# Performance work log

Hardware: AMD Instinct MI355X
Metric: run time of the kernel (lower is better)

The kernel has to match this reference:

```python
import jax, jax.numpy as jnp
import numpy as np

B, N, D = 4, 2048, 2048
HEADS, KV_HEADS = 16, 4
DH = D // HEADS            # 128 per-head dim
KV_RATIO = HEADS // KV_HEADS
MAX_LEN, MAX_BSZ = 2048, 4
EPS = 1.1920929e-07        # torch.finfo(float32).eps (RMSNorm default eps=None)


def _rot_tables(n, d, base=10000.0):
    thetas = base ** (-jnp.arange(0, d, 2, dtype=jnp.float32) / d)   # [d/2]
    ang = jnp.arange(n, dtype=jnp.float32)[:, None] * thetas[None, :]
    cos = jnp.repeat(jnp.cos(ang), 2, axis=-1)   # [n, d] interleaved pairs
    sin = jnp.repeat(jnp.sin(ang), 2, axis=-1)
    return cos, sin


def _rotate_half_inverted(x):
    x1 = x[..., ::2]
    x2 = x[..., 1::2]
    return jnp.stack([-x2, x1], axis=-1).reshape(x.shape)


def _apply_rotation(x, end, start=0):
    cos, sin = _rot_tables(MAX_LEN, DH)
    return x * cos[start:end] + _rotate_half_inverted(x) * sin[start:end]


def setup_inputs() -> dict:
    key = jax.random.key(0)
    ks = jax.random.split(key, 4)
    s = 0.02
    return {
        "x": jax.random.normal(ks[0], (B, N, D), jnp.float32),
        "norm_w": jnp.ones((D,), jnp.float32),
        "qw": jax.random.normal(ks[1], (HEADS * DH, D), jnp.float32) * s,
        "qb": jnp.zeros((HEADS * DH,), jnp.float32),
        "kvw": jax.random.normal(ks[2], (2 * DH * KV_HEADS, D), jnp.float32) * s,
        "kvb": jnp.zeros((2 * DH * KV_HEADS,), jnp.float32),
        "wow": jax.random.normal(ks[3], (D, HEADS * DH), jnp.float32) * s,
        "wob": jnp.zeros((D,), jnp.float32),
        "kv_cache": jnp.zeros((MAX_BSZ, MAX_LEN, 2 * DH * KV_HEADS), jnp.float32),
        "pos": 0,
    }


def reference(x, norm_w, qw, qb, kvw, kvb, wow, wob, kv_cache, pos):
    b, n, d = x.shape
    t = pos + n  # total cached length
    # RMSNorm
    xn = x * jax.lax.rsqrt(jnp.mean(x * x, axis=-1, keepdims=True) + EPS) * norm_w
    # Q projection -> [b, heads, n, dh]
    q = (xn @ qw.T + qb).reshape(b, n, HEADS, DH).transpose(0, 2, 1, 3)
    # KV projection + cache write/read
    kv = xn @ kvw.T + kvb                                  # [b, n, 2*dh*kv_heads]
    cache = jax.lax.dynamic_update_slice(kv_cache, kv, (0, pos, 0))
    kvf = cache[:b, :t].reshape(b, t, KV_HEADS, 2 * DH).transpose(0, 2, 1, 3)
    kvf = jnp.repeat(kvf, KV_RATIO, axis=1)                # GQA expand -> [b, heads, t, 2dh]
    k, v = kvf[..., :DH], kvf[..., DH:]
    # RoPE (interleaved-pair variant)
    q = _apply_rotation(q, t, pos)
    k = _apply_rotation(k, t, 0)
    # Attention (decoder causal)
    attn = jnp.einsum("bhqd,bhkd->bhqk", q, k) / jnp.sqrt(jnp.float32(DH))
    if n > 1:
        mask = jnp.triu(jnp.ones((n, t), bool), k=1 + pos)
        attn = jnp.where(mask, -jnp.inf, attn)
    attn = jax.nn.softmax(attn, axis=-1)
    o = jnp.einsum("bhqk,bhkd->bhqd", attn, v).transpose(0, 2, 1, 3).reshape(b, n, HEADS * DH)
    return o @ wow.T + wob
```

## Files before the change

### kernel.cpp

```cpp
#include <hip/hip_runtime.h>
#include <hip/hip_bf16.h>

typedef unsigned short u16;
typedef unsigned int u32;
typedef __attribute__((ext_vector_type(4))) float f32x4;
typedef __attribute__((ext_vector_type(8))) short s16x8;

#define B_ 4
#define N_ 2048
#define D_ 2048
#define HEADS_ 16
#define KVH_ 4
#define DH_ 128
#define KVD_ 1024
#define M_ 8192
#define SCALE_ 0.08838834764831845f

__device__ __forceinline__ u16 f2bf(float f) {
  u32 u = __builtin_bit_cast(u32, f);
  return (u16)((u + 0x7FFFu + ((u >> 16) & 1u)) >> 16);
}

__device__ __forceinline__ void gload_lds16(const void* g, void* l) {
  __builtin_amdgcn_global_load_lds(
      (const __attribute__((address_space(1))) u32*)g,
      (__attribute__((address_space(3))) u32*)l, 16, 0, 0);
}

__global__ __launch_bounds__(256)
void rope_tab_k(float* __restrict__ cost, float* __restrict__ sint)
{
  const int idx = blockIdx.x * 256 + threadIdx.x;
  const int p = idx >> 6, i = idx & 63;
  const float theta = expf(-(float)i * 0.015625f * 9.210340371976184f);
  float s, c;
  sincosf((float)p * theta, &s, &c);
  cost[idx] = c;
  sint[idx] = s;
}

__global__ __launch_bounds__(256)
void cvt_bf16_k(const float* __restrict__ s, u16* __restrict__ d, int n)
{
  const int i = (blockIdx.x * 256 + threadIdx.x) * 8;
  if (i >= n) return;
  const f32x4 a = *(const f32x4*)(s + i);
  const f32x4 b = *(const f32x4*)(s + i + 4);
  s16x8 o;
  #pragma unroll
  for (int j = 0; j < 4; ++j) { o[j] = (short)f2bf(a[j]); o[4 + j] = (short)f2bf(b[j]); }
  *(s16x8*)(d + i) = o;
}

__global__ __launch_bounds__(256)
void rmsnorm_k(const float* __restrict__ x, const float* __restrict__ w, u16* __restrict__ xn)
{
  const int row = blockIdx.x, t = threadIdx.x;
  const float* xr = x + (size_t)row * D_;
  const f32x4 a = *(const f32x4*)(xr + t * 8);
  const f32x4 b = *(const f32x4*)(xr + t * 8 + 4);
  float ss = a[0]*a[0] + a[1]*a[1] + a[2]*a[2] + a[3]*a[3]
           + b[0]*b[0] + b[1]*b[1] + b[2]*b[2] + b[3]*b[3];
  #pragma unroll
  for (int off = 32; off >= 1; off >>= 1) ss += __shfl_xor(ss, off);
  __shared__ float wss[4];
  if ((t & 63) == 0) wss[t >> 6] = ss;
  __syncthreads();
  const float tot = wss[0] + wss[1] + wss[2] + wss[3];
  const float rs = rsqrtf(tot * (1.0f / D_) + 1.1920929e-07f);
  s16x8 o;
  #pragma unroll
  for (int j = 0; j < 4; ++j) {
    o[j]     = (short)f2bf(a[j] * rs * w[t * 8 + j]);
    o[4 + j] = (short)f2bf(b[j] * rs * w[t * 8 + 4 + j]);
  }
  *(s16x8*)(xn + (size_t)row * D_ + t * 8) = o;
}

template<int EPI>
__global__ __launch_bounds__(256)
void gemm_bt(const u16* __restrict__ A, const u16* __restrict__ Bw,
             void* __restrict__ Cv, const float* __restrict__ bias,
             int N, int K,
             const float* __restrict__ cos_t, const float* __restrict__ sin_t)
{
  __shared__ u16 As[128 * 32];
  __shared__ u16 Bs[128 * 32];
  const int t = threadIdx.x;
  const int w = t >> 6, lane = t & 63;
  const int g = lane >> 4, lr = lane & 15;
  const int row0 = blockIdx.x * 128, col0 = blockIdx.y * 128;
  const int wr = (w >> 1) * 64, wc = (w & 1) * 64;

  f32x4 acc[4][4] = {};

  const u16* gA = A + (size_t)(row0 + w * 16 + (lane >> 2)) * K + (lane & 3) * 8;
  const u16* gB = Bw + (size_t)(col0 + w * 16 + (lane >> 2)) * K + (lane & 3) * 8;
  u16* lA = As + (w * 16) * 32;
  u16* lB = Bs + (w * 16) * 32;

  for (int kt = 0; kt < K; kt += 32) {
    #pragma unroll
    for (int r = 0; r < 2; ++r) {
      gload_lds16(gA + (size_t)(r * 64) * K + kt, lA + r * 64 * 32);
      gload_lds16(gB + (size_t)(r * 64) * K + kt, lB + r * 64 * 32);
    }
    __syncthreads();
    s16x8 af[4], bf[4];
    #pragma unroll
    for (int i = 0; i < 4; ++i) {
      af[i] = *(const s16x8*)(As + (wr + i * 16 + lr) * 32 + g * 8);
      bf[i] = *(const s16x8*)(Bs + (wc + i * 16 + lr) * 32 + g * 8);
    }
    #pragma unroll
    for (int mi = 0; mi < 4; ++mi)
      #pragma unroll
      for (int ni = 0; ni < 4; ++ni)
        acc[mi][ni] = __builtin_amdgcn_mfma_f32_16x16x32_bf16(af[mi], bf[ni], acc[mi][ni], 0, 0, 0);
    __syncthreads();
  }

  #pragma unroll
  for (int mi = 0; mi < 4; ++mi) {
    #pragma unroll
    for (int ni = 0; ni < 4; ++ni) {
      const int cc = col0 + wc + ni * 16 + lr;
      const float bv = bias[cc];
      #pragma unroll
      for (int j = 0; j < 4; ++j) {
        const int rr = row0 + wr + mi * 16 + g * 4 + j;
        float v = acc[mi][ni][j] + bv;
        if (EPI == 0) {
          ((float*)Cv)[(size_t)rr * N + cc] = v;
        } else if (EPI == 1) {
          ((u16*)Cv)[(size_t)rr * N + cc] = f2bf(v);
        } else if (EPI == 2) {
          const int pos = rr & (N_ - 1);
          const int d = cc & (DH_ - 1);
          const float pv = __shfl_xor(v, 1);
          const float c = cos_t[pos * 64 + (d >> 1)];
          const float s = sin_t[pos * 64 + (d >> 1)];
          const float o = (d & 1) ? fmaf(v, c, pv * s) : fmaf(v, c, -pv * s);
          ((u16*)Cv)[(size_t)rr * N + cc] = f2bf(o);
        } else {
          const int pos = rr & (N_ - 1);
          const int dm = cc & 255;
          const float pv = __shfl_xor(v, 1);
          float o = v;
          if (dm < DH_) {
            const float c = cos_t[pos * 64 + (dm >> 1)];
            const float s = sin_t[pos * 64 + (dm >> 1)];
            o = (dm & 1) ? fmaf(v, c, pv * s) : fmaf(v, c, -pv * s);
          }
          ((u16*)Cv)[(size_t)rr * N + cc] = f2bf(o);
        }
      }
    }
  }
}

__global__ __launch_bounds__(256)
void vtrans_k(const u16* __restrict__ kvb, u16* __restrict__ vt)
{
  __shared__ u16 tile[64][65];
  const int z = blockIdx.z, b = z >> 2, kh = z & 3;
  const int p0 = blockIdx.x * 64, d0 = blockIdx.y * 64;
  const int t = threadIdx.x;
  #pragma unroll
  for (int r = 0; r < 2; ++r) {
    const int pl = r * 32 + (t >> 3), dl = (t & 7) * 8;
    const s16x8 v = *(const s16x8*)(kvb + (size_t)(b * N_ + p0 + pl) * KVD_ + kh * 256 + 128 + d0 + dl);
    #pragma unroll
    for (int jj = 0; jj < 8; ++jj) tile[pl][dl + jj] = (u16)v[jj];
  }
  __syncthreads();
  #pragma unroll
  for (int r = 0; r < 2; ++r) {
    const int dl = r * 32 + (t >> 3), pl = (t & 7) * 8;
    s16x8 o;
    #pragma unroll
    for (int jj = 0; jj < 8; ++jj) o[jj] = (short)tile[pl + jj][dl];
    *(s16x8*)(vt + ((size_t)(z * DH_ + d0 + dl)) * N_ + p0 + pl) = o;
  }
}

__global__ __launch_bounds__(512, 2)
void attn_k(const u16* __restrict__ q, const u16* __restrict__ kvb,
            const u16* __restrict__ vt, u16* __restrict__ out)
{
  const int fi = blockIdx.x, h = blockIdx.y, b = blockIdx.z;
  const int kh = h >> 2;
  const int t = threadIdx.x, w = t >> 6, lane = t & 63;
  const int g = lane >> 4, lr = lane & 15;

  __shared__ __align__(16) u16 Ks[2][64 * 128];
  __shared__ __align__(16) u16 Vs[2][128 * 64];
  __shared__ __align__(16) u16 Ps[8][16 * 64];

  const int kc = 2 * w;
  const int kr0 = kc * 4 + (lane >> 4);
  const int ksw0 = (lane & 15) ^ (kr0 & 7);
  const int kr1 = kr0 + 4;
  const int ksw1 = (lane & 15) ^ (kr1 & 7);
  const int vd0 = kc * 8 + (lane >> 3);
  const int vsw0 = (lane & 7) ^ (vd0 & 7);
  const int vd1 = vd0 + 8;
  const int vsw1 = (lane & 7) ^ (vd1 & 7);

  const u16* kbase = kvb + (size_t)b * (N_ * KVD_) + kh * 256;
  const u16* vbase = vt + (size_t)((b * KVH_ + kh) * DH_) * N_;

  int cur = 0;

  auto issue = [&](int kt, int buf) {
    gload_lds16(kbase + (size_t)(kt * 64 + kr0) * KVD_ + ksw0 * 8, &Ks[buf][kc * 512]);
    gload_lds16(kbase + (size_t)(kt * 64 + kr1) * KVD_ + ksw1 * 8, &Ks[buf][(kc + 1) * 512]);
    gload_lds16(vbase + (size_t)vd0 * N_ + kt * 64 + vsw0 * 8, &Vs[buf][kc * 512]);
    gload_lds16(vbase + (size_t)vd1 * N_ + kt * 64 + vsw1 * 8, &Vs[buf][(kc + 1) * 512]);
  };

  auto run_qtile = [&](int qi, int nkt, bool chain) {
    const int qrow0 = qi * 128 + w * 16;
    s16x8 qf[4];
    {
      const u16* qp = q + (size_t)(b * N_ + qrow0 + lr) * D_ + h * DH_;
      #pragma unroll
      for (int ks = 0; ks < 4; ++ks) qf[ks] = *(const s16x8*)(qp + ks * 32 + g * 8);
    }
    f32x4 o_acc[8] = {};
    float m_j[4], l_j[4];
    #pragma unroll
    for (int j = 0; j < 4; ++j) { m_j[j] = -1e30f; l_j[j] = 0.0f; }

    for (int kt = 0; kt < nkt; ++kt) {
      __syncthreads();
      if (kt + 1 < nkt)      issue(kt + 1, cur ^ 1);
      else if (chain)        issue(0, cur ^ 1);

      const u16* Kc = &Ks[cur][0];
      const u16* Vc = &Vs[cur][0];

      f32x4 sf[4] = {};
      #pragma unroll
      for (int ks = 0; ks < 4; ++ks) {
        #pragma unroll
        for (int kvf = 0; kvf < 4; ++kvf) {
          const int kvr = kvf * 16 + lr;
          const int ba = (kvr * 256 + ks * 64 + g * 16) ^ ((kvr & 7) << 4);
          const s16x8 kf = *(const s16x8*)((const char*)Kc + ba);
          sf[kvf] = __builtin_amdgcn_mfma_f32_16x16x32_bf16(qf[ks], kf, sf[kvf], 0, 0, 0);
        }
      }

      float pfac[4];
      #pragma unroll
      for (int j = 0; j < 4; ++j) {
        float mx = m_j[j];
        #pragma unroll
        for (int kvf = 0; kvf < 4; ++kvf) {
          float sv = sf[kvf][j] * SCALE_;
          const int kj = kt * 64 + kvf * 16 + lr;
          const int qi_row = qrow0 + g * 4 + j;
          if (kj > qi_row) sv = -1e30f;
          sf[kvf][j] = sv;
          mx = fmaxf(mx, sv);
        }
        mx = fmaxf(mx, __shfl_xor(mx, 1));
        mx = fmaxf(mx, __shfl_xor(mx, 2));
        mx = fmaxf(mx, __shfl_xor(mx, 4));
        mx = fmaxf(mx, __shfl_xor(mx, 8));
        pfac[j] = __expf(m_j[j] - mx);
        m_j[j] = mx;
      }
      #pragma unroll
      for (int df = 0; df < 8; ++df)
        #pragma unroll
        for (int j = 0; j < 4; ++j) o_acc[df][j] *= pfac[j];
      #pragma unroll
      for (int j = 0; j < 4; ++j) {
        float sum = 0.0f;
        #pragma unroll
        for (int kvf = 0; kvf < 4; ++kvf) {
          const float p = __expf(sf[kvf][j] - m_j[j]);
          sf[kvf][j] = p;
          sum += p;
        }
        sum += __shfl_xor(sum, 1);
        sum += __shfl_xor(sum, 2);
        sum += __shfl_xor(sum, 4);
        sum += __shfl_xor(sum, 8);
        l_j[j] = l_j[j] * pfac[j] + sum;
      }

      #pragma unroll
      for (int kvf = 0; kvf < 4; ++kvf)
        #pragma unroll
        for (int j = 0; j < 4; ++j) {
          const int rq = g * 4 + j, ck = kvf * 16 + lr;
          const int ba = (rq * 128 + ck * 2) ^ ((rq & 7) << 4);
          *(u16*)((char*)&Ps[w][0] + ba) = f2bf(sf[kvf][j]);
        }

      #pragma unroll
      for (int kk = 0; kk < 2; ++kk) {
        const int bap = (lr * 128 + kk * 64 + g * 16) ^ ((lr & 7) << 4);
        const s16x8 pf = *(const s16x8*)((const char*)&Ps[w][0] + bap);
        #pragma unroll
        for (int df = 0; df < 8; ++df) {
          const int dd = df * 16 + lr;
          const int bav = (dd * 128 + kk * 64 + g * 16) ^ ((dd & 7) << 4);
          const s16x8 vf = *(const s16x8*)((const char*)Vc + bav);
          o_acc[df] = __builtin_amdgcn_mfma_f32_16x16x32_bf16(pf, vf, o_acc[df], 0, 0, 0);
        }
      }
      cur ^= 1;
    }

    float inv_l[4];
    #pragma unroll
    for (int j = 0; j < 4; ++j) inv_l[j] = 1.0f / l_j[j];
    u16* op = out + (size_t)(b * N_ + qrow0) * D_ + h * DH_;
    #pragma unroll
    for (int df = 0; df < 8; ++df)
      #pragma unroll
      for (int j = 0; j < 4; ++j)
        op[(size_t)(g * 4 + j) * D_ + df * 16 + lr] = f2bf(o_acc[df][j] * inv_l[j]);
  };

  const int qlo = fi, qhi = 15 - fi;
  issue(0, 0);
  run_qtile(qlo, 2 * qlo + 2, true);
  run_qtile(qhi, 2 * qhi + 2, false);
}

extern "C" void kernel_launch(void* const* d_in, const int* in_sizes, int n_in,
                              void* d_out, int out_size, void* d_ws, size_t ws_size,
                              hipStream_t stream) {
  const float* x      = (const float*)d_in[0];
  const float* normw  = (const float*)d_in[1];
  const float* qw     = (const float*)d_in[2];
  const float* qbias  = (const float*)d_in[3];
  const float* kvw    = (const float*)d_in[4];
  const float* kvbias = (const float*)d_in[5];
  const float* wow    = (const float*)d_in[6];
  const float* wob    = (const float*)d_in[7];
  float* out = (float*)d_out;

  char* ws = (char*)d_ws;
  u16* xn    = (u16*)(ws + 0);
  u16* dq    = (u16*)(ws + 33554432);
  u16* dkv   = (u16*)(ws + 67108864);
  u16* dvt   = (u16*)(ws + 83886080);
  u16* qwb   = (u16*)(ws + 92274688);
  u16* kvwb  = (u16*)(ws + 100663296);
  u16* wowb  = (u16*)(ws + 104857600);
  float* cost = (float*)(ws + 113246208);
  float* sint = (float*)(ws + 113770496);

  rope_tab_k<<<512, 256, 0, stream>>>(cost, sint);
  cvt_bf16_k<<<2048, 256, 0, stream>>>(qw, qwb, 2048 * 2048);
  cvt_bf16_k<<<1024, 256, 0, stream>>>(kvw, kvwb, 1024 * 2048);
  cvt_bf16_k<<<2048, 256, 0, stream>>>(wow, wowb, 2048 * 2048);
  rmsnorm_k<<<8192, 256, 0, stream>>>(x, normw, xn);
  gemm_bt<2><<<dim3(64, 16), 256, 0, stream>>>(xn, qwb, (void*)dq, qbias, 2048, 2048, cost, sint);
  gemm_bt<3><<<dim3(64, 8), 256, 0, stream>>>(xn, kvwb, (void*)dkv, kvbias, 1024, 2048, cost, sint);
  vtrans_k<<<dim3(32, 2, 16), 256, 0, stream>>>(dkv, dvt);
  attn_k<<<dim3(8, 16, 4), 512, 0, stream>>>(dq, dkv, dvt, xn);
  gemm_bt<0><<<dim3(64, 16), 256, 0, stream>>>(xn, wowb, (void*)out, wob, 2048, 2048, nullptr, nullptr);
}
```

Baseline: 495.5 us.

## Fuse Q and KV projections into one GEMM and streamline attention softmax

```diff
diff --git a/kernel.cpp b/kernel.cpp
--- a/kernel.cpp
+++ b/kernel.cpp
@@ -15,10 +15,19 @@
 #define KVD_ 1024
 #define M_ 8192
 #define SCALE_ 0.08838834764831845f
+#define QSCALE2_ 0.12753257518622628f
 
 __device__ __forceinline__ u16 f2bf(float f) {
   u32 u = __builtin_bit_cast(u32, f);
   return (u16)((u + 0x7FFFu + ((u >> 16) & 1u)) >> 16);
+}
+
+__device__ __forceinline__ float fexp2(float x) {
+#if __has_builtin(__builtin_amdgcn_exp2f)
+  return __builtin_amdgcn_exp2f(x);
+#else
+  return exp2f(x);
+#endif
 }
 
 __device__ __forceinline__ void gload_lds16(const void* g, void* l) {
@@ -80,7 +89,8 @@
 template<int EPI>
 __global__ __launch_bounds__(256)
 void gemm_bt(const u16* __restrict__ A, const u16* __restrict__ Bw,
-             void* __restrict__ Cv, const float* __restrict__ bias,
+             void* __restrict__ Cv, void* __restrict__ Cv2,
+             const float* __restrict__ bias, const float* __restrict__ bias2,
              int N, int K,
              const float* __restrict__ cos_t, const float* __restrict__ sin_t)
 {
@@ -125,34 +135,33 @@
     #pragma unroll
     for (int ni = 0; ni < 4; ++ni) {
       const int cc = col0 + wc + ni * 16 + lr;
-      const float bv = bias[cc];
+      const float bv = (EPI == 4 && cc >= 2048) ? bias2[cc - 2048] : bias[cc];
       #pragma unroll
       for (int j = 0; j < 4; ++j) {
         const int rr = row0 + wr + mi * 16 + g * 4 + j;
         float v = acc[mi][ni][j] + bv;
         if (EPI == 0) {
-          ((float*)Cv)[(size_t)rr * N + cc] = v;
-        } else if (EPI == 1) {
-          ((u16*)Cv)[(size_t)rr * N + cc] = f2bf(v);
-        } else if (EPI == 2) {
-          const int pos = rr & (N_ - 1);
-          const int d = cc & (DH_ - 1);
-          const float pv = __shfl_xor(v, 1);
-          const float c = cos_t[pos * 64 + (d >> 1)];
-          const float s = sin_t[pos * 64 + (d >> 1)];
-          const float o = (d & 1) ? fmaf(v, c, pv * s) : fmaf(v, c, -pv * s);
-          ((u16*)Cv)[(size_t)rr * N + cc] = f2bf(o);
+          ((float*)Cv)[(size_t)rr * 2048 + cc] = v;
         } else {
           const int pos = rr & (N_ - 1);
-          const int dm = cc & 255;
           const float pv = __shfl_xor(v, 1);
-          float o = v;
-          if (dm < DH_) {
-            const float c = cos_t[pos * 64 + (dm >> 1)];
-            const float s = sin_t[pos * 64 + (dm >> 1)];
-            o = (dm & 1) ? fmaf(v, c, pv * s) : fmaf(v, c, -pv * s);
-          }
-          ((u16*)Cv)[(size_t)rr * N + cc] = f2bf(o);
+          if (cc < 2048) {
+            const int d = cc & (DH_ - 1);
+            const float c = cos_t[pos * 64 + (d >> 1)];
+            const float s = sin_t[pos * 64 + (d >> 1)];
+            const float o = (cc & 1) ? fmaf(v, c, pv * s) : fmaf(v, c, -pv * s);
+            ((u16*)Cv)[(size_t)rr * 2048 + cc] = f2bf(o);
+          } else {
+            const int ccc = cc - 2048;
+            const int dm = ccc & 255;
+            float o = v;
+            if (dm < DH_) {
+              const float c = cos_t[pos * 64 + (dm >> 1)];
+              const float s = sin_t[pos * 64 + (dm >> 1)];
+              o = (dm & 1) ? fmaf(v, c, pv * s) : fmaf(v, c, -pv * s);
+            }
+            ((u16*)Cv2)[(size_t)rr * 1024 + ccc] = f2bf(o);
+          }
         }
       }
     }
@@ -221,6 +230,7 @@
 
   auto run_qtile = [&](int qi, int nkt, bool chain) {
     const int qrow0 = qi * 128 + w * 16;
+    const int td = qrow0 >> 6;
     s16x8 qf[4];
     {
       const u16* qp = q + (size_t)(b * N_ + qrow0 + lr) * D_ + h * DH_;
@@ -237,88 +247,103 @@
       if (kt + 1 < nkt)      issue(kt + 1, cur ^ 1);
       else if (chain)        issue(0, cur ^ 1);
 
-      const u16* Kc = &Ks[cur][0];
-      const u16* Vc = &Vs[cur][0];
-
-      f32x4 sf[4] = {};
-      #pragma unroll
-      for (int ks = 0; ks < 4; ++ks) {
+      if (kt <= td) {
+        const u16* Kc = &Ks[cur][0];
+        const u16* Vc = &Vs[cur][0];
+
+        f32x4 sf[4] = {};
+        __builtin_amdgcn_s_setprio(1);
         #pragma unroll
-        for (int kvf = 0; kvf < 4; ++kvf) {
-          const int kvr = kvf * 16 + lr;
-          const int ba = (kvr * 256 + ks * 64 + g * 16) ^ ((kvr & 7) << 4);
-          const s16x8 kf = *(const s16x8*)((const char*)Kc + ba);
-          sf[kvf] = __builtin_amdgcn_mfma_f32_16x16x32_bf16(qf[ks], kf, sf[kvf], 0, 0, 0);
-        }
-      }
-
-      float pfac[4];
-      #pragma unroll
-      for (int j = 0; j < 4; ++j) {
-        float mx = m_j[j];
-        #pragma unroll
-        for (int kvf = 0; kvf < 4; ++kvf) {
-          float sv = sf[kvf][j] * SCALE_;
-          const int kj = kt * 64 + kvf * 16 + lr;
-          const int qi_row = qrow0 + g * 4 + j;
-          if (kj > qi_row) sv = -1e30f;
-          sf[kvf][j] = sv;
-          mx = fmaxf(mx, sv);
-        }
-        mx = fmaxf(mx, __shfl_xor(mx, 1));
-        mx = fmaxf(mx, __shfl_xor(mx, 2));
-        mx = fmaxf(mx, __shfl_xor(mx, 4));
-        mx = fmaxf(mx, __shfl_xor(mx, 8));
-        pfac[j] = __expf(m_j[j] - mx);
-        m_j[j] = mx;
-      }
-      #pragma unroll
-      for (int df = 0; df < 8; ++df)
-        #pragma unroll
-        for (int j = 0; j < 4; ++j) o_acc[df][j] *= pfac[j];
-      #pragma unroll
-      for (int j = 0; j < 4; ++j) {
-        float sum = 0.0f;
-        #pragma unroll
-        for (int kvf = 0; kvf < 4; ++kvf) {
-          const float p = __expf(sf[kvf][j] - m_j[j]);
-          sf[kvf][j] = p;
-          sum += p;
-        }
-        sum += __shfl_xor(sum, 1);
-        sum += __shfl_xor(sum, 2);
-        sum += __shfl_xor(sum, 4);
-        sum += __shfl_xor(sum, 8);
-        l_j[j] = l_j[j] * pfac[j] + sum;
-      }
-
-      #pragma unroll
-      for (int kvf = 0; kvf < 4; ++kvf)
+        for (int ks = 0; ks < 4; ++ks) {
+          #pragma unroll
+          for (int kvf = 0; kvf < 4; ++kvf) {
+            const int kvr = kvf * 16 + lr;
+            const int ba = (kvr * 256 + ks * 64 + g * 16) ^ ((kvr & 7) << 4);
+            const s16x8 kf = *(const s16x8*)((const char*)Kc + ba);
+            sf[kvf] = __builtin_amdgcn_mfma_f32_16x16x32_bf16(qf[ks], kf, sf[kvf], 0, 0, 0);
+          }
+        }
+        __builtin_amdgcn_s_setprio(0);
+
+        const bool need_mask = (kt == td);
+        float pmax[4];
         #pragma unroll
         for (int j = 0; j < 4; ++j) {
-          const int rq = g * 4 + j, ck = kvf * 16 + lr;
-          const int ba = (rq * 128 + ck * 2) ^ ((rq & 7) << 4);
-          *(u16*)((char*)&Ps[w][0] + ba) = f2bf(sf[kvf][j]);
-        }
-
-      #pragma unroll
-      for (int kk = 0; kk < 2; ++kk) {
-        const int bap = (lr * 128 + kk * 64 + g * 16) ^ ((lr & 7) << 4);
-        const s16x8 pf = *(const s16x8*)((const char*)&Ps[w][0] + bap);
+          float mx = -1e30f;
+          #pragma unroll
+          for (int kvf = 0; kvf < 4; ++kvf) {
+            float sv = sf[kvf][j] * QSCALE2_;
+            if (need_mask) {
+              const int kj = kt * 64 + kvf * 16 + lr;
+              const int qi_row = qrow0 + g * 4 + j;
+              if (kj > qi_row) sv = -1e30f;
+            }
+            sf[kvf][j] = sv;
+            mx = fmaxf(mx, sv);
+          }
+          mx = fmaxf(mx, __shfl_xor(mx, 1));
+          mx = fmaxf(mx, __shfl_xor(mx, 2));
+          mx = fmaxf(mx, __shfl_xor(mx, 4));
+          mx = fmaxf(mx, __shfl_xor(mx, 8));
+          pmax[j] = mx;
+        }
+
+        const float needv = fmaxf(fmaxf(pmax[0] - m_j[0], pmax[1] - m_j[1]),
+                                  fmaxf(pmax[2] - m_j[2], pmax[3] - m_j[3]));
+        if (__any(needv > 8.0f)) {
+          #pragma unroll
+          for (int j = 0; j < 4; ++j) {
+            const float mn = fmaxf(m_j[j], pmax[j]);
+            const float pf = fexp2(m_j[j] - mn);
+            m_j[j] = mn;
+            l_j[j] *= pf;
+            #pragma unroll
+            for (int df = 0; df < 8; ++df) o_acc[df][j] *= pf;
+          }
+        }
+
         #pragma unroll
-        for (int df = 0; df < 8; ++df) {
-          const int dd = df * 16 + lr;
-          const int bav = (dd * 128 + kk * 64 + g * 16) ^ ((dd & 7) << 4);
-          const s16x8 vf = *(const s16x8*)((const char*)Vc + bav);
-          o_acc[df] = __builtin_amdgcn_mfma_f32_16x16x32_bf16(pf, vf, o_acc[df], 0, 0, 0);
-        }
+        for (int j = 0; j < 4; ++j) {
+          float lacc = 0.0f;
+          #pragma unroll
+          for (int kvf = 0; kvf < 4; ++kvf) {
+            const float p = fexp2(sf[kvf][j] - m_j[j]);
+            lacc += p;
+            const int rq = g * 4 + j, ck = kvf * 16 + lr;
+            const int ba = (rq * 128 + ck * 2) ^ ((rq & 7) << 4);
+            *(u16*)((char*)&Ps[w][0] + ba) = (u16)(__builtin_bit_cast(u32, p) >> 16);
+          }
+          l_j[j] += lacc;
+        }
+
+        __builtin_amdgcn_s_setprio(1);
+        #pragma unroll
+        for (int kk = 0; kk < 2; ++kk) {
+          const int bap = (lr * 128 + kk * 64 + g * 16) ^ ((lr & 7) << 4);
+          const s16x8 pf = *(const s16x8*)((const char*)&Ps[w][0] + bap);
+          #pragma unroll
+          for (int df = 0; df < 8; ++df) {
+            const int dd = df * 16 + lr;
+            const int bav = (dd * 128 + kk * 64 + g * 16) ^ ((dd & 7) << 4);
+            const s16x8 vf = *(const s16x8*)((const char*)Vc + bav);
+            o_acc[df] = __builtin_amdgcn_mfma_f32_16x16x32_bf16(pf, vf, o_acc[df], 0, 0, 0);
+          }
+        }
+        __builtin_amdgcn_s_setprio(0);
       }
       cur ^= 1;
     }
 
     float inv_l[4];
     #pragma unroll
-    for (int j = 0; j < 4; ++j) inv_l[j] = 1.0f / l_j[j];
+    for (int j = 0; j < 4; ++j) {
+      float s4 = l_j[j];
+      s4 += __shfl_xor(s4, 1);
+      s4 += __shfl_xor(s4, 2);
+      s4 += __shfl_xor(s4, 4);
+      s4 += __shfl_xor(s4, 8);
+      inv_l[j] = 1.0f / s4;
+    }
     u16* op = out + (size_t)(b * N_ + qrow0) * D_ + h * DH_;
     #pragma unroll
     for (int df = 0; df < 8; ++df)
@@ -351,20 +376,20 @@
   u16* dq    = (u16*)(ws + 33554432);
   u16* dkv   = (u16*)(ws + 67108864);
   u16* dvt   = (u16*)(ws + 83886080);
-  u16* qwb   = (u16*)(ws + 92274688);
-  u16* kvwb  = (u16*)(ws + 100663296);
+  u16* wqkv  = (u16*)(ws + 92274688);
   u16* wowb  = (u16*)(ws + 104857600);
   float* cost = (float*)(ws + 113246208);
   float* sint = (float*)(ws + 113770496);
 
   rope_tab_k<<<512, 256, 0, stream>>>(cost, sint);
-  cvt_bf16_k<<<2048, 256, 0, stream>>>(qw, qwb, 2048 * 2048);
-  cvt_bf16_k<<<1024, 256, 0, stream>>>(kvw, kvwb, 1024 * 2048);
+  cvt_bf16_k<<<2048, 256, 0, stream>>>(qw, wqkv, 2048 * 2048);
+  cvt_bf16_k<<<1024, 256, 0, stream>>>(kvw, wqkv + 2048 * 2048, 1024 * 2048);
   cvt_bf16_k<<<2048, 256, 0, stream>>>(wow, wowb, 2048 * 2048);
   rmsnorm_k<<<8192, 256, 0, stream>>>(x, normw, xn);
-  gemm_bt<2><<<dim3(64, 16), 256, 0, stream>>>(xn, qwb, (void*)dq, qbias, 2048, 2048, cost, sint);
-  gemm_bt<3><<<dim3(64, 8), 256, 0, stream>>>(xn, kvwb, (void*)dkv, kvbias, 1024, 2048, cost, sint);
+  gemm_bt<4><<<dim3(64, 24), 256, 0, stream>>>(xn, wqkv, (void*)dq, (void*)dkv,
+                                               qbias, kvbias, 3072, 2048, cost, sint);
   vtrans_k<<<dim3(32, 2, 16), 256, 0, stream>>>(dkv, dvt);
   attn_k<<<dim3(8, 16, 4), 512, 0, stream>>>(dq, dkv, dvt, xn);
-  gemm_bt<0><<<dim3(64, 16), 256, 0, stream>>>(xn, wowb, (void*)out, wob, 2048, 2048, nullptr, nullptr);
-}
+  gemm_bt<0><<<dim3(64, 16), 256, 0, stream>>>(xn, wowb, (void*)out, nullptr,
+                                               wob, nullptr, 2048, 2048, nullptr, nullptr);
+}
```

After: 461.6 us. -6.8%, faster.
